# Kernel tuning notes

Measured on AMD Instinct MI355X. Metric: run time of the kernel, lower is better.

The kernel has to match this reference:

```python
import jax, jax.numpy as jnp
import numpy as np

Q = 3
PAD = 4
STRIDE = 1
DIL = 1
MAX_SHIFT = 4.0


def setup_inputs() -> dict:
    key = jax.random.key(0)
    k1, k2, k3, k4 = jax.random.split(key, 4)
    B, Cin, L, Cout, K = 16, 128, 8192, 128, 9
    x = jax.random.normal(k1, (B, Cin, L), jnp.float32)
    # shifts stored pre-divided by max_shift (as in reset_parameters); y-shift zeroed
    sx = jax.random.uniform(k2, (Cin, 1), jnp.float32, minval=-0.5, maxval=0.5)
    shifts = jnp.concatenate([sx, jnp.zeros((Cin, 1), jnp.float32)], axis=1)
    weights = jax.random.normal(k3, (Cout, Q * Cin, K), jnp.float32) * 0.02
    bias = jax.random.normal(k4, (Cout,), jnp.float32) * 0.01
    return {"x": x, "weights": weights, "bias": bias, "shifts": shifts}


def _channel_shift(x, shift):
    # x: [B, C, L]; shift: [C]. Equivalent to affine_grid+grid_sample with H=1,
    # align_corners=False, zeros padding: output[i] = lerp(x, i + shift).
    B, C, L = x.shape
    pos = jnp.arange(L, dtype=x.dtype)[None, :] + shift[:, None]  # [C, L]
    i0 = jnp.floor(pos).astype(jnp.int32)
    i1 = i0 + 1
    w1 = (pos - i0.astype(x.dtype))[None]  # [1, C, L]

    def gather(idx):
        valid = ((idx >= 0) & (idx < L)).astype(x.dtype)[None]  # zeros padding
        idx_b = jnp.broadcast_to(jnp.clip(idx, 0, L - 1)[None], x.shape)
        return jnp.take_along_axis(x, idx_b, axis=2) * valid

    return gather(i0) * (1.0 - w1) + gather(i1) * w1


def reference(x, weights, bias, shifts):
    xs = _channel_shift(x, shifts[:, 0] * MAX_SHIFT)  # [B, C, L]
    # q-order power expansion along channels: [x, x^2, ..., x^q]
    xq = jnp.concatenate([xs ** i for i in range(1, Q + 1)], axis=1)  # [B, q*C, L]
    out = jax.lax.conv_general_dilated(
        xq, weights,
        window_strides=(STRIDE,), padding=[(PAD, PAD)],
        rhs_dilation=(DIL,), dimension_numbers=("NCH", "OIH", "NCH"))
    return out + bias[None, :, None]
```

## Files before the change

### kernel.cpp

```cpp
#include <hip/hip_runtime.h>


#define B_    16
#define CIN   128
#define L_    8192
#define COUT  128
#define K_    9
#define QMAX  3
#define KQ    (QMAX * CIN)
#define KTOT  (K_ * KQ)
#define BK    64
#define GUARD 4
#define LROWS (L_ + 2 * GUARD)
#define XQOFF (1u << 20)

typedef __attribute__((ext_vector_type(8)))  short bf16x8;
typedef __attribute__((ext_vector_type(16))) float f32x16;
typedef __attribute__((ext_vector_type(4)))  int   int4v;

__device__ __forceinline__ unsigned short f2bf(float v) {
    union { float f; unsigned u; } cv; cv.f = v;
    unsigned u = cv.u;
    return (unsigned short)((u + 0x7FFFu + ((u >> 16) & 1u)) >> 16);
}

__global__ __launch_bounds__(256) void prep_weights(
    const float* __restrict__ w, unsigned short* __restrict__ wa)
{
    int g = blockIdx.x * 256 + threadIdx.x;
    if (g >= COUT * KTOT) return;
    const int c   = g >> 13;
    const int r   = g & 8191;
    const int co  = r >> 6;
    const int s8  = (r >> 3) & 7;
    const int i   = r & 7;
    const int kk  = ((s8 ^ (co & 7)) << 3) | i;
    const int k   = c * BK + kk;
    const int tap = k / KQ;
    const int qc  = k - tap * KQ;
    wa[g] = f2bf(w[((size_t)co * KQ + qc) * K_ + tap]);
}

__global__ __launch_bounds__(256) void xq_prep(
    const float* __restrict__ x, const float* __restrict__ shifts,
    unsigned short* __restrict__ xq)
{
    __shared__ float xtile[128 * 65];
    __shared__ unsigned short tile[32 * KQ];
    const int l0   = blockIdx.x * 32;
    const int b    = blockIdx.y;
    const int tid  = threadIdx.x;
    const int lane = tid & 63;
    const int w    = tid >> 6;
    const float* xb = x + (size_t)b * CIN * L_;

    const int col = l0 - 4 + lane;
    const bool cok = (col >= 0) & (col < L_);
    const float* xsrc = xb + col;
    float rv[32];
#pragma unroll
    for (int j = 0; j < 32; ++j)
        rv[j] = cok ? xsrc[(size_t)(j * 4 + w) * L_] : 0.0f;
#pragma unroll
    for (int j = 0; j < 32; ++j)
        xtile[(j * 4 + w) * 65 + lane] = rv[j];
    __syncthreads();

    {
        const int ci   = tid & 127;
        const int lgrp = tid >> 7;
        const float sh = shifts[2 * ci] * 4.0f;
        const float fl = floorf(sh);
        const int  ifl = (int)fl;
        const float w1 = sh - fl;
        int c0 = lgrp * 16 + 4 + ifl;
        float v_prev = xtile[ci * 65 + c0];
#pragma unroll
        for (int j = 0; j < 16; ++j) {
            const int ll = lgrp * 16 + j;
            const float v_next = xtile[ci * 65 + c0 + 1];
            const float xs = fmaf(w1, v_next - v_prev, v_prev);
            const float x2 = xs * xs;
            const float x3 = x2 * xs;
            tile[ll * KQ + ci]       = f2bf(xs);
            tile[ll * KQ + 128 + ci] = f2bf(x2);
            tile[ll * KQ + 256 + ci] = f2bf(x3);
            v_prev = v_next;
            ++c0;
        }
    }
    __syncthreads();

    const int4v* src = (const int4v*)tile;
    int4v* dst = (int4v*)(xq + ((size_t)b * LROWS + l0 + GUARD) * KQ);
#pragma unroll
    for (int it = 0; it < 6; ++it)
        dst[it * 256 + tid] = src[it * 256 + tid];

    if (blockIdx.x == 0) {
        int4v* g0 = (int4v*)(xq + (size_t)b * LROWS * KQ);
        if (tid < 192) g0[tid] = (int4v){0, 0, 0, 0};
    }
    if (blockIdx.x == gridDim.x - 1) {
        int4v* g1 = (int4v*)(xq + ((size_t)b * LROWS + L_ + GUARD) * KQ);
        if (tid < 192) g1[tid] = (int4v){0, 0, 0, 0};
    }
}

__global__ __launch_bounds__(256, 4) void gemm(
    const unsigned short* __restrict__ wa,
    const unsigned short* __restrict__ xq,
    const float*          __restrict__ bias,
    float*                __restrict__ out)
{
    __shared__ __align__(16) unsigned short ldsA[COUT * BK];
    __shared__ __align__(16) unsigned short ldsB[136 * BK];

    const int l0   = blockIdx.x * 128;
    const int b    = blockIdx.y;
    const int tid  = threadIdx.x;
    const int lane = tid & 63;
    const int w    = tid >> 6;
    const int cobase = (w >> 1) * 64;
    const int nbase  = (w & 1) * 64;
    const int n5 = lane & 31;
    const int h  = lane >> 5;

    const int bj_row = lane >> 3;
    const size_t bLaneOff = (size_t)bj_row * KQ + (size_t)(((lane & 7) ^ (bj_row & 7)) << 3);

    int aaddr[2][4];
#pragma unroll
    for (int fi = 0; fi < 2; ++fi)
#pragma unroll
        for (int kc = 0; kc < 4; ++kc) {
            const int ar = cobase + fi * 32 + n5;
            aaddr[fi][kc] = ar * 128 + ((((kc << 1) | h) ^ (ar & 7)) << 4);
        }

    f32x16 acc[2][2];
#pragma unroll
    for (int i = 0; i < 2; ++i)
#pragma unroll
        for (int j = 0; j < 2; ++j) acc[i][j] = (f32x16){};

    const unsigned short* xqb   = xq + (size_t)b * LROWS * KQ;
    const unsigned short* bbase = xqb + (size_t)l0 * KQ + bLaneOff;

#pragma unroll 1
    for (int s = 0; s < 6; ++s) {
        const unsigned short* bsrc = bbase + s * 64;
#pragma unroll
        for (int i = 0; i < 4; ++i) {
            const int g = w * 4 + i;
            __builtin_amdgcn_global_load_lds(
                (const __attribute__((address_space(1))) void*)(bsrc + (size_t)g * 8 * KQ),
                (__attribute__((address_space(3))) void*)((char*)ldsB + g * 1024),
                16, 0, 0);
        }
        if (w == 0)
            __builtin_amdgcn_global_load_lds(
                (const __attribute__((address_space(1))) void*)(bsrc + (size_t)16 * 8 * KQ),
                (__attribute__((address_space(3))) void*)((char*)ldsB + 16 * 1024),
                16, 0, 0);

#pragma unroll 1
        for (int tap = 0; tap < K_; ++tap) {
            const int c = tap * 6 + s;
            const unsigned short* agsrc = wa + (size_t)c * 8192 + (size_t)(w * 4) * 512 + lane * 8;
#pragma unroll
            for (int i = 0; i < 4; ++i)
                __builtin_amdgcn_global_load_lds(
                    (const __attribute__((address_space(1))) void*)(agsrc + i * 512),
                    (__attribute__((address_space(3))) void*)((char*)ldsA + (w * 4 + i) * 1024),
                    16, 0, 0);
            __syncthreads();
#pragma unroll
            for (int kc = 0; kc < 4; ++kc) {
                const int br0 = tap + nbase + n5;
                const int ba0 = br0 * 128 + ((((kc << 1) | h) ^ (br0 & 7)) << 4);
                const int ba1 = ba0 + 32 * 128;
                const bf16x8 a0 = *(const bf16x8*)((const char*)ldsA + aaddr[0][kc]);
                const bf16x8 a1 = *(const bf16x8*)((const char*)ldsA + aaddr[1][kc]);
                const bf16x8 b0 = *(const bf16x8*)((const char*)ldsB + ba0);
                const bf16x8 b1 = *(const bf16x8*)((const char*)ldsB + ba1);
                acc[0][0] = __builtin_amdgcn_mfma_f32_32x32x16_bf16(a0, b0, acc[0][0], 0, 0, 0);
                acc[0][1] = __builtin_amdgcn_mfma_f32_32x32x16_bf16(a0, b1, acc[0][1], 0, 0, 0);
                acc[1][0] = __builtin_amdgcn_mfma_f32_32x32x16_bf16(a1, b0, acc[1][0], 0, 0, 0);
                acc[1][1] = __builtin_amdgcn_mfma_f32_32x32x16_bf16(a1, b1, acc[1][1], 0, 0, 0);
            }
            __syncthreads();
        }
    }

#pragma unroll
    for (int fi = 0; fi < 2; ++fi)
#pragma unroll
        for (int bj = 0; bj < 2; ++bj)
#pragma unroll
            for (int r = 0; r < 16; ++r) {
                const int co = cobase + fi * 32 + (r & 3) + 8 * (r >> 2) + 4 * h;
                const int l  = l0 + nbase + bj * 32 + n5;
                out[((size_t)(b * COUT + co)) * L_ + l] = acc[fi][bj][r] + bias[co];
            }
}

extern "C" void kernel_launch(void* const* d_in, const int* in_sizes, int n_in,
                              void* d_out, int out_size, void* d_ws, size_t ws_size,
                              hipStream_t stream) {
    const float* x      = (const float*)d_in[0];
    const float* w      = (const float*)d_in[1];
    const float* bias   = (const float*)d_in[2];
    const float* shifts = (const float*)d_in[3];
    float* out = (float*)d_out;

    const size_t need = (size_t)XQOFF + (size_t)B_ * LROWS * KQ * 2;
    if (ws_size < need) return;

    unsigned short* wa = (unsigned short*)d_ws;
    unsigned short* xq = (unsigned short*)((char*)d_ws + XQOFF);

    const int nw = COUT * KTOT;
    prep_weights<<<(nw + 255) / 256, 256, 0, stream>>>(w, wa);

    dim3 gq(L_ / 32, B_);
    xq_prep<<<gq, 256, 0, stream>>>(x, shifts, xq);

    dim3 gg(L_ / 128, B_);
    gemm<<<gg, 256, 0, stream>>>(wa, xq, bias, out);
}
```

Baseline: 257.9 us.

## Double-buffer weight tiles in GEMM and prefetch next stage during MFMA

The GEMM kernel now keeps two LDS buffers for the weight tile. While the MFMAs run on the current tap, it issues global-to-LDS loads for the next tap, and the next input-channel slab of B is loaded right after the last tap of each stage. Explicit vmcnt waits, raw s_barrier and setprio replace the paired __syncthreads, so load latency can hide behind compute. The extra A buffer raises LDS use, so the occupancy hint drops from 4 to 3 blocks. Separately, xq_prep shrinks its staging tile to the 41 columns it actually needs, cutting LDS use and skipping unused stores.

```diff
diff --git a/kernel.cpp b/kernel.cpp
--- a/kernel.cpp
+++ b/kernel.cpp
@@ -13,6 +13,7 @@
 #define GUARD 4
 #define LROWS (L_ + 2 * GUARD)
 #define XQOFF (1u << 20)
+#define XT    41
 
 typedef __attribute__((ext_vector_type(8)))  short bf16x8;
 typedef __attribute__((ext_vector_type(16))) float f32x16;
@@ -41,11 +42,11 @@
     wa[g] = f2bf(w[((size_t)co * KQ + qc) * K_ + tap]);
 }
 
-__global__ __launch_bounds__(256) void xq_prep(
+__global__ __launch_bounds__(256, 3) void xq_prep(
     const float* __restrict__ x, const float* __restrict__ shifts,
     unsigned short* __restrict__ xq)
 {
-    __shared__ float xtile[128 * 65];
+    __shared__ float xtile[128 * XT];
     __shared__ unsigned short tile[32 * KQ];
     const int l0   = blockIdx.x * 32;
     const int b    = blockIdx.y;
@@ -55,15 +56,17 @@
     const float* xb = x + (size_t)b * CIN * L_;
 
     const int col = l0 - 4 + lane;
-    const bool cok = (col >= 0) & (col < L_);
+    const bool cok = (lane < XT) & (col >= 0) & (col < L_);
     const float* xsrc = xb + col;
     float rv[32];
 #pragma unroll
     for (int j = 0; j < 32; ++j)
         rv[j] = cok ? xsrc[(size_t)(j * 4 + w) * L_] : 0.0f;
-#pragma unroll
-    for (int j = 0; j < 32; ++j)
-        xtile[(j * 4 + w) * 65 + lane] = rv[j];
+    if (lane < XT) {
+#pragma unroll
+        for (int j = 0; j < 32; ++j)
+            xtile[(j * 4 + w) * XT + lane] = rv[j];
+    }
     __syncthreads();
 
     {
@@ -74,11 +77,11 @@
         const int  ifl = (int)fl;
         const float w1 = sh - fl;
         int c0 = lgrp * 16 + 4 + ifl;
-        float v_prev = xtile[ci * 65 + c0];
+        float v_prev = xtile[ci * XT + c0];
 #pragma unroll
         for (int j = 0; j < 16; ++j) {
             const int ll = lgrp * 16 + j;
-            const float v_next = xtile[ci * 65 + c0 + 1];
+            const float v_next = xtile[ci * XT + c0 + 1];
             const float xs = fmaf(w1, v_next - v_prev, v_prev);
             const float x2 = xs * xs;
             const float x3 = x2 * xs;
@@ -107,13 +110,13 @@
     }
 }
 
-__global__ __launch_bounds__(256, 4) void gemm(
+__global__ __launch_bounds__(256, 3) void gemm(
     const unsigned short* __restrict__ wa,
     const unsigned short* __restrict__ xq,
     const float*          __restrict__ bias,
     float*                __restrict__ out)
 {
-    __shared__ __align__(16) unsigned short ldsA[COUT * BK];
+    __shared__ __align__(16) unsigned short ldsA[2][COUT * BK];
     __shared__ __align__(16) unsigned short ldsB[136 * BK];
 
     const int l0   = blockIdx.x * 128;
@@ -146,10 +149,10 @@
 
     const unsigned short* xqb   = xq + (size_t)b * LROWS * KQ;
     const unsigned short* bbase = xqb + (size_t)l0 * KQ + bLaneOff;
-
-#pragma unroll 1
-    for (int s = 0; s < 6; ++s) {
-        const unsigned short* bsrc = bbase + s * 64;
+    const unsigned short* aw    = wa + (size_t)(w * 4) * 512 + (size_t)lane * 8;
+
+    {
+        const unsigned short* bsrc = bbase;
 #pragma unroll
         for (int i = 0; i < 4; ++i) {
             const int g = w * 4 + i;
@@ -163,25 +166,48 @@
                 (const __attribute__((address_space(1))) void*)(bsrc + (size_t)16 * 8 * KQ),
                 (__attribute__((address_space(3))) void*)((char*)ldsB + 16 * 1024),
                 16, 0, 0);
-
+        const unsigned short* agsrc = aw;
+#pragma unroll
+        for (int i = 0; i < 4; ++i)
+            __builtin_amdgcn_global_load_lds(
+                (const __attribute__((address_space(1))) void*)(agsrc + i * 512),
+                (__attribute__((address_space(3))) void*)((char*)ldsA[0] + (w * 4 + i) * 1024),
+                16, 0, 0);
+    }
+    __syncthreads();
+
+#pragma unroll 1
+    for (int s = 0; s < 6; ++s) {
 #pragma unroll 1
         for (int tap = 0; tap < K_; ++tap) {
-            const int c = tap * 6 + s;
-            const unsigned short* agsrc = wa + (size_t)c * 8192 + (size_t)(w * 4) * 512 + lane * 8;
-#pragma unroll
-            for (int i = 0; i < 4; ++i)
-                __builtin_amdgcn_global_load_lds(
-                    (const __attribute__((address_space(1))) void*)(agsrc + i * 512),
-                    (__attribute__((address_space(3))) void*)((char*)ldsA + (w * 4 + i) * 1024),
-                    16, 0, 0);
-            __syncthreads();
+            const int par  = (s + tap) & 1;
+            const bool last = (s == 5) && (tap == 8);
+
+            if (!last) {
+                const int cn = (tap < 8) ? ((tap + 1) * 6 + s) : (s + 1);
+                const unsigned short* agsrc = aw + (size_t)cn * 8192;
+                char* adst = (char*)ldsA[par ^ 1];
+#pragma unroll
+                for (int i = 0; i < 4; ++i)
+                    __builtin_amdgcn_global_load_lds(
+                        (const __attribute__((address_space(1))) void*)(agsrc + i * 512),
+                        (__attribute__((address_space(3))) void*)(adst + (w * 4 + i) * 1024),
+                        16, 0, 0);
+            }
+            if (last) asm volatile("s_waitcnt vmcnt(0)" ::: "memory");
+            else      asm volatile("s_waitcnt vmcnt(4)" ::: "memory");
+            __builtin_amdgcn_s_barrier();
+            __builtin_amdgcn_sched_barrier(0);
+
+            __builtin_amdgcn_s_setprio(1);
+            const char* Ab = (const char*)ldsA[par];
 #pragma unroll
             for (int kc = 0; kc < 4; ++kc) {
                 const int br0 = tap + nbase + n5;
                 const int ba0 = br0 * 128 + ((((kc << 1) | h) ^ (br0 & 7)) << 4);
                 const int ba1 = ba0 + 32 * 128;
-                const bf16x8 a0 = *(const bf16x8*)((const char*)ldsA + aaddr[0][kc]);
-                const bf16x8 a1 = *(const bf16x8*)((const char*)ldsA + aaddr[1][kc]);
+                const bf16x8 a0 = *(const bf16x8*)(Ab + aaddr[0][kc]);
+                const bf16x8 a1 = *(const bf16x8*)(Ab + aaddr[1][kc]);
                 const bf16x8 b0 = *(const bf16x8*)((const char*)ldsB + ba0);
                 const bf16x8 b1 = *(const bf16x8*)((const char*)ldsB + ba1);
                 acc[0][0] = __builtin_amdgcn_mfma_f32_32x32x16_bf16(a0, b0, acc[0][0], 0, 0, 0);
@@ -189,7 +215,28 @@
                 acc[1][0] = __builtin_amdgcn_mfma_f32_32x32x16_bf16(a1, b0, acc[1][0], 0, 0, 0);
                 acc[1][1] = __builtin_amdgcn_mfma_f32_32x32x16_bf16(a1, b1, acc[1][1], 0, 0, 0);
             }
-            __syncthreads();
+            __builtin_amdgcn_s_setprio(0);
+            __builtin_amdgcn_sched_barrier(0);
+            __builtin_amdgcn_s_barrier();
+            __builtin_amdgcn_sched_barrier(0);
+
+            if (tap == 8 && s < 5) {
+                const unsigned short* bsrc = bbase + (s + 1) * 64;
+#pragma unroll
+                for (int i = 0; i < 4; ++i) {
+                    const int g = w * 4 + i;
+                    __builtin_amdgcn_global_load_lds(
+                        (const __attribute__((address_space(1))) void*)(bsrc + (size_t)g * 8 * KQ),
+                        (__attribute__((address_space(3))) void*)((char*)ldsB + g * 1024),
+                        16, 0, 0);
+                }
+                if (w == 0)
+                    __builtin_amdgcn_global_load_lds(
+                        (const __attribute__((address_space(1))) void*)(bsrc + (size_t)16 * 8 * KQ),
+                        (__attribute__((address_space(3))) void*)((char*)ldsB + 16 * 1024),
+                        16, 0, 0);
+                __builtin_amdgcn_sched_barrier(0);
+            }
         }
     }
 
```

Measured after the change: 273.2 us. +5.9%, slower.

## Load weight fragments directly to registers with prefetch, dropping LDS A staging

Applied to the files above, without the earlier changes.

The GEMM no longer stages the weight tile through LDS with per-tap barriers. Each wave reads its bf16 A fragments straight from global memory (L2-resident, unswizzled layout) into registers and prefetches the next tap's fragments while the current MFMAs run, which removes two __syncthreads per tap. The cost is more VGPR pressure, so the occupancy hint drops to 3 waves per SIMD, and each wave now issues redundant global reads of A. xq_prep also trims its shared x tile from 65 to 41 columns to cut LDS use and wasted loads.

```diff
diff --git a/kernel.cpp b/kernel.cpp
--- a/kernel.cpp
+++ b/kernel.cpp
@@ -13,6 +13,7 @@
 #define GUARD 4
 #define LROWS (L_ + 2 * GUARD)
 #define XQOFF (1u << 20)
+#define XT    41
 
 typedef __attribute__((ext_vector_type(8)))  short bf16x8;
 typedef __attribute__((ext_vector_type(16))) float f32x16;
@@ -32,20 +33,18 @@
     const int c   = g >> 13;
     const int r   = g & 8191;
     const int co  = r >> 6;
-    const int s8  = (r >> 3) & 7;
-    const int i   = r & 7;
-    const int kk  = ((s8 ^ (co & 7)) << 3) | i;
+    const int kk  = r & 63;
     const int k   = c * BK + kk;
     const int tap = k / KQ;
     const int qc  = k - tap * KQ;
     wa[g] = f2bf(w[((size_t)co * KQ + qc) * K_ + tap]);
 }
 
-__global__ __launch_bounds__(256) void xq_prep(
+__global__ __launch_bounds__(256, 3) void xq_prep(
     const float* __restrict__ x, const float* __restrict__ shifts,
     unsigned short* __restrict__ xq)
 {
-    __shared__ float xtile[128 * 65];
+    __shared__ float xtile[128 * XT];
     __shared__ unsigned short tile[32 * KQ];
     const int l0   = blockIdx.x * 32;
     const int b    = blockIdx.y;
@@ -55,15 +54,17 @@
     const float* xb = x + (size_t)b * CIN * L_;
 
     const int col = l0 - 4 + lane;
-    const bool cok = (col >= 0) & (col < L_);
+    const bool cok = (lane < XT) & (col >= 0) & (col < L_);
     const float* xsrc = xb + col;
     float rv[32];
 #pragma unroll
     for (int j = 0; j < 32; ++j)
         rv[j] = cok ? xsrc[(size_t)(j * 4 + w) * L_] : 0.0f;
-#pragma unroll
-    for (int j = 0; j < 32; ++j)
-        xtile[(j * 4 + w) * 65 + lane] = rv[j];
+    if (lane < XT) {
+#pragma unroll
+        for (int j = 0; j < 32; ++j)
+            xtile[(j * 4 + w) * XT + lane] = rv[j];
+    }
     __syncthreads();
 
     {
@@ -74,11 +75,11 @@
         const int  ifl = (int)fl;
         const float w1 = sh - fl;
         int c0 = lgrp * 16 + 4 + ifl;
-        float v_prev = xtile[ci * 65 + c0];
+        float v_prev = xtile[ci * XT + c0];
 #pragma unroll
         for (int j = 0; j < 16; ++j) {
             const int ll = lgrp * 16 + j;
-            const float v_next = xtile[ci * 65 + c0 + 1];
+            const float v_next = xtile[ci * XT + c0 + 1];
             const float xs = fmaf(w1, v_next - v_prev, v_prev);
             const float x2 = xs * xs;
             const float x3 = x2 * xs;
@@ -107,13 +108,12 @@
     }
 }
 
-__global__ __launch_bounds__(256, 4) void gemm(
+__global__ __launch_bounds__(256, 3) void gemm(
     const unsigned short* __restrict__ wa,
     const unsigned short* __restrict__ xq,
     const float*          __restrict__ bias,
     float*                __restrict__ out)
 {
-    __shared__ __align__(16) unsigned short ldsA[COUT * BK];
     __shared__ __align__(16) unsigned short ldsB[136 * BK];
 
     const int l0   = blockIdx.x * 128;
@@ -129,15 +129,6 @@
     const int bj_row = lane >> 3;
     const size_t bLaneOff = (size_t)bj_row * KQ + (size_t)(((lane & 7) ^ (bj_row & 7)) << 3);
 
-    int aaddr[2][4];
-#pragma unroll
-    for (int fi = 0; fi < 2; ++fi)
-#pragma unroll
-        for (int kc = 0; kc < 4; ++kc) {
-            const int ar = cobase + fi * 32 + n5;
-            aaddr[fi][kc] = ar * 128 + ((((kc << 1) | h) ^ (ar & 7)) << 4);
-        }
-
     f32x16 acc[2][2];
 #pragma unroll
     for (int i = 0; i < 2; ++i)
@@ -146,6 +137,8 @@
 
     const unsigned short* xqb   = xq + (size_t)b * LROWS * KQ;
     const unsigned short* bbase = xqb + (size_t)l0 * KQ + bLaneOff;
+    const unsigned short* a0p = wa + (size_t)(cobase + n5) * 64 + h * 8;
+    const unsigned short* a1p = a0p + 32 * 64;
 
 #pragma unroll 1
     for (int s = 0; s < 6; ++s) {
@@ -164,33 +157,50 @@
                 (__attribute__((address_space(3))) void*)((char*)ldsB + 16 * 1024),
                 16, 0, 0);
 
+        const unsigned short* cp0 = a0p + (size_t)s * 8192;
+        const unsigned short* cp1 = a1p + (size_t)s * 8192;
+        bf16x8 A0[2][4];
+#pragma unroll
+        for (int kc = 0; kc < 4; ++kc) {
+            A0[0][kc] = *(const bf16x8*)(cp0 + kc * 16);
+            A0[1][kc] = *(const bf16x8*)(cp1 + kc * 16);
+        }
+
+        __syncthreads();
+
 #pragma unroll 1
         for (int tap = 0; tap < K_; ++tap) {
-            const int c = tap * 6 + s;
-            const unsigned short* agsrc = wa + (size_t)c * 8192 + (size_t)(w * 4) * 512 + lane * 8;
-#pragma unroll
-            for (int i = 0; i < 4; ++i)
-                __builtin_amdgcn_global_load_lds(
-                    (const __attribute__((address_space(1))) void*)(agsrc + i * 512),
-                    (__attribute__((address_space(3))) void*)((char*)ldsA + (w * 4 + i) * 1024),
-                    16, 0, 0);
-            __syncthreads();
+            bf16x8 A1[2][4];
+            if (tap < 8) {
+                const unsigned short* np0 = a0p + (size_t)((tap + 1) * 6 + s) * 8192;
+                const unsigned short* np1 = np0 + 32 * 64;
+#pragma unroll
+                for (int kc = 0; kc < 4; ++kc) {
+                    A1[0][kc] = *(const bf16x8*)(np0 + kc * 16);
+                    A1[1][kc] = *(const bf16x8*)(np1 + kc * 16);
+                }
+            }
 #pragma unroll
             for (int kc = 0; kc < 4; ++kc) {
                 const int br0 = tap + nbase + n5;
                 const int ba0 = br0 * 128 + ((((kc << 1) | h) ^ (br0 & 7)) << 4);
                 const int ba1 = ba0 + 32 * 128;
-                const bf16x8 a0 = *(const bf16x8*)((const char*)ldsA + aaddr[0][kc]);
-                const bf16x8 a1 = *(const bf16x8*)((const char*)ldsA + aaddr[1][kc]);
                 const bf16x8 b0 = *(const bf16x8*)((const char*)ldsB + ba0);
                 const bf16x8 b1 = *(const bf16x8*)((const char*)ldsB + ba1);
-                acc[0][0] = __builtin_amdgcn_mfma_f32_32x32x16_bf16(a0, b0, acc[0][0], 0, 0, 0);
-                acc[0][1] = __builtin_amdgcn_mfma_f32_32x32x16_bf16(a0, b1, acc[0][1], 0, 0, 0);
-                acc[1][0] = __builtin_amdgcn_mfma_f32_32x32x16_bf16(a1, b0, acc[1][0], 0, 0, 0);
-                acc[1][1] = __builtin_amdgcn_mfma_f32_32x32x16_bf16(a1, b1, acc[1][1], 0, 0, 0);
-            }
-            __syncthreads();
-        }
+                acc[0][0] = __builtin_amdgcn_mfma_f32_32x32x16_bf16(A0[0][kc], b0, acc[0][0], 0, 0, 0);
+                acc[0][1] = __builtin_amdgcn_mfma_f32_32x32x16_bf16(A0[0][kc], b1, acc[0][1], 0, 0, 0);
+                acc[1][0] = __builtin_amdgcn_mfma_f32_32x32x16_bf16(A0[1][kc], b0, acc[1][0], 0, 0, 0);
+                acc[1][1] = __builtin_amdgcn_mfma_f32_32x32x16_bf16(A0[1][kc], b1, acc[1][1], 0, 0, 0);
+            }
+            if (tap < 8) {
+#pragma unroll
+                for (int kc = 0; kc < 4; ++kc) {
+                    A0[0][kc] = A1[0][kc];
+                    A0[1][kc] = A1[1][kc];
+                }
+            }
+        }
+        __syncthreads();
     }
 
 #pragma unroll
```

Measured after the change: 347.4 us. 34.7% more time.
